# Performance work log

Measured on AMD Instinct MI355X. Metric: run time of the kernel, lower is better.

Reference implementation:

```python
import jax, jax.numpy as jnp
import numpy as np

C = 64       # class_number (from json groups)
D = 256      # out_dimension = predicted.shape[1]
N = 262144   # batch size


def setup_inputs() -> dict:
    key = jax.random.key(0)
    k1, k2, k3, k4 = jax.random.split(key, 4)
    predicted = jax.random.normal(k1, (N, D), dtype=jnp.float32)
    target = jax.random.randint(k2, (N,), 0, C)
    centroids = jax.random.normal(k3, (C, D), dtype=jnp.float32)
    # accumulated per-class distance sums are nonnegative (sqrt is applied)
    distances = jax.random.uniform(k4, (C, 1), dtype=jnp.float32) * float(N)
    # count = bincount(target) as the torch module accumulates; clamp >= 1
    ones = jnp.ones((N,), jnp.float32)
    count = jnp.maximum(jax.ops.segment_sum(ones, target, num_segments=C), 1.0)[:, None]
    # build_class_weight_matrix: single group containing every label -> all 1.5
    class_weights = jnp.full((C, C), 1.5, dtype=jnp.float32)
    return dict(predicted=predicted, centroids=centroids, distances=distances,
                count=count, class_weights=class_weights, target=target)


def reference(predicted, centroids, distances, count, class_weights, target):
    # === calculate_loss path (epoch % 3 == 2) ===
    C_ = centroids.shape[0]
    sel_counts = count[target]            # [N,1] gather
    sel_centroids = centroids[target]     # [N,D] gather
    pr = predicted / sel_counts           # [N,D]
    cent_new = centroids.at[target].add(pr)                 # scatter-add
    vec = jnp.linalg.norm(sel_centroids - pr, axis=1)       # [N]
    s = distances.at[target].add(vec[:, None])              # scatter-add [C,1]
    s = jnp.sqrt(s) / count                                 # [C,1]
    # cdist(cent_new, cent_new, p=2) via the norm trick
    sq = jnp.sum(cent_new * cent_new, axis=1)               # [C]
    d2 = jnp.maximum(sq[:, None] + sq[None, :] - 2.0 * (cent_new @ cent_new.T), 0.0)
    mask = ~jnp.eye(C_, dtype=bool)
    m = jnp.sqrt(jnp.where(mask, d2, 1.0))                  # safe off-diagonal sqrt
    S = s + s.T                                             # s[i] + s[j], [C,C]
    term = jnp.where(mask, class_weights * S / m, 0.0)
    sum_ = jnp.sum(term)
    loss = sum_ / C_ * (C_ - 1)
    return loss + jnp.sum(jnp.abs(cent_new)) / 1000000.0
```

## Files before the change

kernel.cpp:

```cpp
#include <hip/hip_runtime.h>
#include <math.h>

#define NROWS 262144
#define DIM   256
#define NC    64
#define CD    (NC*DIM)
#define NBLK  512

#define OFF_CENT   0
#define OFF_ABS    16384
#define OFF_PAIR   16896
#define OFF_SPART  16960
#define OFF_SST2   49728
#define OFF_PART   50752

typedef short  bf16x8 __attribute__((ext_vector_type(8)));
typedef float  f32x16 __attribute__((ext_vector_type(16)));

#define DPP_ADD(v, ctrl) \
    ((v) + __int_as_float(__builtin_amdgcn_update_dpp(0, __float_as_int(v), (ctrl), 0xf, 0xf, true)))

__device__ __forceinline__ float dpp_sum64(float v) {
    v = DPP_ADD(v, 0x111);
    v = DPP_ADD(v, 0x112);
    v = DPP_ADD(v, 0x114);
    v = DPP_ADD(v, 0x118);
    v = DPP_ADD(v, 0x142);
    v = DPP_ADD(v, 0x143);
    return v;
}

__device__ __forceinline__ unsigned int bf16rne2(float lo, float hi) {
    unsigned int ul = __float_as_uint(lo);
    ul = (ul + 0x7FFFu + ((ul >> 16) & 1u)) >> 16;
    unsigned int uh = __float_as_uint(hi);
    uh = (uh + 0x7FFFu + ((uh >> 16) & 1u)) & 0xFFFF0000u;
    return ul | uh;
}
__device__ __forceinline__ unsigned short bf16rne1(float v) {
    unsigned int x = __float_as_uint(v);
    return (unsigned short)((x + 0x7FFFu + ((x >> 16) & 1u)) >> 16);
}
__device__ __forceinline__ float bflo(unsigned int u) { return __uint_as_float(u << 16); }
__device__ __forceinline__ float bfhi(unsigned int u) { return __uint_as_float(u & 0xFFFF0000u); }
__device__ __forceinline__ float bfup(unsigned short u) { return __uint_as_float(((unsigned int)u) << 16); }

__device__ __forceinline__ void do_mfma_chunk(const unsigned short* pb,
                                              const int* tgts, int rbase,
                                              int lane, int d0,
                                              f32x16& a0r, f32x16& a1r)
{
    const int g8  = (lane >> 5) << 3;
    const int cA  = lane & 31;
    const int cB  = 32 + cA;
    const int col = d0 + cA;
    #pragma unroll
    for (int ks = 0; ks < 4; ++ks) {
        const int rA = rbase + ks * 16 + g8;
        const int t0 = tgts[rA+0], t1 = tgts[rA+1], t2 = tgts[rA+2], t3 = tgts[rA+3];
        const int t4 = tgts[rA+4], t5 = tgts[rA+5], t6 = tgts[rA+6], t7 = tgts[rA+7];
        union { unsigned int u[4]; bf16x8 v; } A0, A1, B;
        A0.u[0] = ((t0==cA)?0x3F80u:0u) | (((t1==cA)?0x3F80u:0u) << 16);
        A0.u[1] = ((t2==cA)?0x3F80u:0u) | (((t3==cA)?0x3F80u:0u) << 16);
        A0.u[2] = ((t4==cA)?0x3F80u:0u) | (((t5==cA)?0x3F80u:0u) << 16);
        A0.u[3] = ((t6==cA)?0x3F80u:0u) | (((t7==cA)?0x3F80u:0u) << 16);
        A1.u[0] = ((t0==cB)?0x3F80u:0u) | (((t1==cB)?0x3F80u:0u) << 16);
        A1.u[1] = ((t2==cB)?0x3F80u:0u) | (((t3==cB)?0x3F80u:0u) << 16);
        A1.u[2] = ((t4==cB)?0x3F80u:0u) | (((t5==cB)?0x3F80u:0u) << 16);
        A1.u[3] = ((t6==cB)?0x3F80u:0u) | (((t7==cB)?0x3F80u:0u) << 16);
        const int kr = ks * 16 + g8;
        #pragma unroll
        for (int p = 0; p < 4; ++p) {
            const unsigned int lo = pb[(kr + 2*p    ) * 256 + col];
            const unsigned int hi = pb[(kr + 2*p + 1) * 256 + col];
            B.u[p] = lo | (hi << 16);
        }
        a0r = __builtin_amdgcn_mfma_f32_32x32x16_bf16(A0.v, B.v, a0r, 0, 0, 0);
        a1r = __builtin_amdgcn_mfma_f32_32x32x16_bf16(A1.v, B.v, a1r, 0, 0, 0);
    }
}

__global__ __launch_bounds__(512, 4)
void k_main(const float* __restrict__ pred, const float* __restrict__ cent,
            const float* __restrict__ count, const int* __restrict__ tgt,
            float* __restrict__ ws)
{
    __shared__ unsigned short pbf[64 * 256];
    __shared__ unsigned short cbf[NC * 256];
    __shared__ int   tgt_s[512];
    __shared__ float inv_s[64];
    __shared__ float vec_s[512];
    __shared__ float sw_s[8][64];

    const int tid  = threadIdx.x;
    const int w    = tid >> 6;
    const int lane = tid & 63;
    const int base = blockIdx.x * 512;

    tgt_s[tid] = tgt[base + tid];
    if (tid < 64) inv_s[tid] = 1.0f / count[tid];
    {
        const float2* c2 = (const float2*)cent;
        unsigned int* cb32 = (unsigned int*)cbf;
        #pragma unroll
        for (int i = 0; i < 16; ++i) {
            const int o = i * 512 + tid;
            const float2 cf = c2[o];
            cb32[o] = bf16rne2(cf.x, cf.y);
        }
    }
    __syncthreads();

    const float4* pred4 = (const float4*)pred;
    const int d0 = w * 32;

    f32x16 acc0 = {};
    f32x16 acc1 = {};

    #pragma unroll 1
    for (int ch = 0; ch < 8; ++ch) {
        const size_t gr = (size_t)(base + ch * 64) * 64 + lane;
        float4 p0 = pred4[gr + (size_t)( 0 + w) * 64];
        float4 p1 = pred4[gr + (size_t)( 8 + w) * 64];
        float4 p2 = pred4[gr + (size_t)(16 + w) * 64];
        float4 p3 = pred4[gr + (size_t)(24 + w) * 64];
        float4 p4 = pred4[gr + (size_t)(32 + w) * 64];
        float4 p5 = pred4[gr + (size_t)(40 + w) * 64];
        float4 p6 = pred4[gr + (size_t)(48 + w) * 64];
        float4 p7 = pred4[gr + (size_t)(56 + w) * 64];

#define ROW(pp, i)                                                             \
        {                                                                      \
            const int rc = 8*(i) + w;                                          \
            const int r  = ch * 64 + rc;                                       \
            const int c  = tgt_s[r];                                           \
            const float iv = inv_s[c];                                         \
            const uint2 cu = *(const uint2*)&cbf[c * 256 + lane * 4];          \
            const float dx = bflo(cu.x) - pp.x * iv;                           \
            const float dy = bfhi(cu.x) - pp.y * iv;                           \
            const float dz = bflo(cu.y) - pp.z * iv;                           \
            const float dw = bfhi(cu.y) - pp.w * iv;                           \
            float ss = dx*dx + dy*dy + dz*dz + dw*dw;                          \
            ss = dpp_sum64(ss);                                                \
            if (lane == 63) vec_s[r] = sqrtf(ss);                              \
            *(uint2*)&pbf[rc * 256 + lane * 4] =                               \
                make_uint2(bf16rne2(pp.x, pp.y), bf16rne2(pp.z, pp.w));        \
        }
        ROW(p0, 0) ROW(p1, 1) ROW(p2, 2) ROW(p3, 3)
        ROW(p4, 4) ROW(p5, 5) ROW(p6, 6) ROW(p7, 7)
#undef ROW
        __syncthreads();
        do_mfma_chunk(pbf, tgt_s, ch * 64, lane, d0, acc0, acc1);
        __syncthreads();
    }

    unsigned short* pp = (unsigned short*)(ws + OFF_PART) + (size_t)blockIdx.x * CD;
    const int dim = d0 + (lane & 31);
    #pragma unroll
    for (int reg = 0; reg < 16; ++reg) {
        const int crow = (reg & 3) + 8 * (reg >> 2) + 4 * (lane >> 5);
        pp[(     crow) * 256 + dim] = bf16rne1(acc0[reg]);
        pp[(32 + crow) * 256 + dim] = bf16rne1(acc1[reg]);
    }

    {
        const float vv = vec_s[w * 64 + lane];
        const int   cc = tgt_s[w * 64 + lane];
        float accs = 0.f;
        for (int k = 0; k < NC; ++k) {
            float sel = (cc == k) ? vv : 0.f;
            sel = dpp_sum64(sel);
            const float tot = __shfl(sel, 63, 64);
            accs += (lane == k) ? tot : 0.f;
        }
        sw_s[w][lane] = accs;
    }
    __syncthreads();
    if (w == 0) {
        float s = 0.f;
        #pragma unroll
        for (int q = 0; q < 8; ++q) s += sw_s[q][lane];
        ws[OFF_SPART + blockIdx.x * 64 + lane] = s;
    }
}

__global__ __launch_bounds__(512)
void k_red2(const float* __restrict__ cent, const float* __restrict__ count,
            float* __restrict__ ws)
{
    __shared__ float red2[16][32];
    __shared__ float absl[32];
    __shared__ float sred[8][64];
    const int b = blockIdx.x, tid = threadIdx.x;

    const int eo = tid & 31;
    const int g  = tid >> 5;
    const int e  = b * 32 + eo;
    const unsigned short* pp = (const unsigned short*)(ws + OFF_PART);
    float s = 0.f;
    const int p0 = g * 32;
    #pragma unroll 8
    for (int p = p0; p < p0 + 32; ++p) s += bfup(pp[(size_t)p * CD + e]);
    red2[g][eo] = s;
    __syncthreads();
    if (tid < 32) {
        float tot = 0.f;
        #pragma unroll
        for (int q = 0; q < 16; ++q) tot += red2[q][tid];
        const int e2 = b * 32 + tid;
        const int c  = e2 >> 8;
        const float val = cent[e2] + tot / count[c];
        ws[OFF_CENT + e2] = val;
        absl[tid] = fabsf(val);
    }
    __syncthreads();
    if (tid < 64) {
        float a = (tid < 32) ? absl[tid] : 0.f;
        a = dpp_sum64(a);
        if (tid == 63) ws[OFF_ABS + b] = a;
    }
    if (b >= 496) {
        const int q  = b - 496;
        const int c  = tid & 63;
        const int rw = tid >> 6;
        float s2 = 0.f;
        #pragma unroll
        for (int i = 0; i < 4; ++i)
            s2 += ws[OFF_SPART + (q * 32 + rw * 4 + i) * 64 + c];
        sred[rw][c] = s2;
        __syncthreads();
        if (tid < 64) {
            float sv = 0.f;
            #pragma unroll
            for (int r = 0; r < 8; ++r) sv += sred[r][tid];
            ws[OFF_SST2 + q * 64 + tid] = sv;
        }
    }
}

__global__ __launch_bounds__(512)
void k_pairs(const float* __restrict__ count, const float* __restrict__ dist,
             const float* __restrict__ cw, float* __restrict__ ws)
{
    __shared__ float sf_s[64];
    __shared__ float wsum[8];
    const int i = blockIdx.x, tid = threadIdx.x;
    const int w = tid >> 6, lane = tid & 63;

    if (tid < 64) {
        float sv = 0.f;
        #pragma unroll
        for (int q = 0; q < 16; ++q) sv += ws[OFF_SST2 + q * 64 + tid];
        sf_s[tid] = sqrtf(dist[tid] + sv) / count[tid];
    }
    __syncthreads();
    const float4* c4 = (const float4*)(ws + OFF_CENT);
    const float si = sf_s[i];
    const float4 ci = c4[i * 64 + lane];
    float acc = 0.f;
    for (int j = w; j < NC; j += 8) {
        if (j == i) continue;
        const float4 cj = c4[j * 64 + lane];
        const float dx = ci.x - cj.x, dy = ci.y - cj.y;
        const float dz = ci.z - cj.z, dw = ci.w - cj.w;
        float ss = dx*dx + dy*dy + dz*dz + dw*dw;
        ss = dpp_sum64(ss);
        if (lane == 63) acc += cw[i * NC + j] * (si + sf_s[j]) / sqrtf(ss);
    }
    if (lane == 63) wsum[w] = acc;
    __syncthreads();
    if (tid == 0) {
        float ps = 0.f;
        #pragma unroll
        for (int q = 0; q < 8; ++q) ps += wsum[q];
        ws[OFF_PAIR + i] = ps;
    }
}

__global__ __launch_bounds__(512)
void k_fin(const float* __restrict__ ws, float* __restrict__ out)
{
    __shared__ float ra[8], rp[8];
    const int tid = threadIdx.x, w = tid >> 6, lane = tid & 63;
    float a = ws[OFF_ABS + tid];
    float p = (tid < 64) ? ws[OFF_PAIR + tid] : 0.f;
    a = dpp_sum64(a);
    p = dpp_sum64(p);
    if (lane == 63) { ra[w] = a; rp[w] = p; }
    __syncthreads();
    if (tid == 0) {
        float as = 0.f, ps = 0.f;
        #pragma unroll
        for (int q = 0; q < 8; ++q) { as += ra[q]; ps += rp[q]; }
        out[0] = ps / 64.0f * 63.0f + as * 1e-6f;
    }
}

extern "C" void kernel_launch(void* const* d_in, const int* in_sizes, int n_in,
                              void* d_out, int out_size, void* d_ws, size_t ws_size,
                              hipStream_t stream)
{
    const float* pred  = (const float*)d_in[0];
    const float* cent  = (const float*)d_in[1];
    const float* dist  = (const float*)d_in[2];
    const float* count = (const float*)d_in[3];
    const float* cw    = (const float*)d_in[4];
    const int*   tgt   = (const int*)d_in[5];
    float* ws  = (float*)d_ws;
    float* out = (float*)d_out;

    k_main <<<NBLK, 512, 0, stream>>>(pred, cent, count, tgt, ws);
    k_red2 <<<NBLK, 512, 0, stream>>>(cent, count, ws);
    k_pairs<<<NC,   512, 0, stream>>>(count, dist, cw, ws);
    k_fin  <<<1,    512, 0, stream>>>(ws, out);
}
```

Before: 75.03 us.

## Double-buffer LDS tiles and prefetch next chunk to overlap loads with MFMA

```diff
diff --git a/kernel.cpp b/kernel.cpp
--- a/kernel.cpp
+++ b/kernel.cpp
@@ -45,17 +45,25 @@
 __device__ __forceinline__ float bfhi(unsigned int u) { return __uint_as_float(u & 0xFFFF0000u); }
 __device__ __forceinline__ float bfup(unsigned short u) { return __uint_as_float(((unsigned int)u) << 16); }
 
-__device__ __forceinline__ void do_mfma_chunk(const unsigned short* pb,
-                                              const int* tgts, int rbase,
-                                              int lane, int d0,
-                                              f32x16& a0r, f32x16& a1r)
+__device__ __forceinline__ void lds_barrier() {
+    __builtin_amdgcn_sched_barrier(0);
+    asm volatile("s_waitcnt lgkmcnt(0)" ::: "memory");
+    __builtin_amdgcn_sched_barrier(0);
+    __builtin_amdgcn_s_barrier();
+    __builtin_amdgcn_sched_barrier(0);
+}
+
+__device__ __forceinline__ void do_mfma_chunk32(const unsigned short* pb,
+                                                const int* tgts, int rbase,
+                                                int lane, int d0,
+                                                f32x16& a0r, f32x16& a1r)
 {
     const int g8  = (lane >> 5) << 3;
     const int cA  = lane & 31;
     const int cB  = 32 + cA;
     const int col = d0 + cA;
     #pragma unroll
-    for (int ks = 0; ks < 4; ++ks) {
+    for (int ks = 0; ks < 2; ++ks) {
         const int rA = rbase + ks * 16 + g8;
         const int t0 = tgts[rA+0], t1 = tgts[rA+1], t2 = tgts[rA+2], t3 = tgts[rA+3];
         const int t4 = tgts[rA+4], t5 = tgts[rA+5], t6 = tgts[rA+6], t7 = tgts[rA+7];
@@ -68,7 +76,7 @@
         A1.u[1] = ((t2==cB)?0x3F80u:0u) | (((t3==cB)?0x3F80u:0u) << 16);
         A1.u[2] = ((t4==cB)?0x3F80u:0u) | (((t5==cB)?0x3F80u:0u) << 16);
         A1.u[3] = ((t6==cB)?0x3F80u:0u) | (((t7==cB)?0x3F80u:0u) << 16);
-        const int kr = ks * 16 + g8;
+        const int kr = (ks * 16 + g8) & 31;
         #pragma unroll
         for (int p = 0; p < 4; ++p) {
             const unsigned int lo = pb[(kr + 2*p    ) * 256 + col];
@@ -85,7 +93,7 @@
             const float* __restrict__ count, const int* __restrict__ tgt,
             float* __restrict__ ws)
 {
-    __shared__ unsigned short pbf[64 * 256];
+    __shared__ unsigned short pbf[2][32 * 256];
     __shared__ unsigned short cbf[NC * 256];
     __shared__ int   tgt_s[512];
     __shared__ float inv_s[64];
@@ -117,22 +125,19 @@
     f32x16 acc0 = {};
     f32x16 acc1 = {};
 
-    #pragma unroll 1
-    for (int ch = 0; ch < 8; ++ch) {
-        const size_t gr = (size_t)(base + ch * 64) * 64 + lane;
-        float4 p0 = pred4[gr + (size_t)( 0 + w) * 64];
-        float4 p1 = pred4[gr + (size_t)( 8 + w) * 64];
-        float4 p2 = pred4[gr + (size_t)(16 + w) * 64];
-        float4 p3 = pred4[gr + (size_t)(24 + w) * 64];
-        float4 p4 = pred4[gr + (size_t)(32 + w) * 64];
-        float4 p5 = pred4[gr + (size_t)(40 + w) * 64];
-        float4 p6 = pred4[gr + (size_t)(48 + w) * 64];
-        float4 p7 = pred4[gr + (size_t)(56 + w) * 64];
-
-#define ROW(pp, i)                                                             \
+    float4 p0, p1, p2, p3;
+
+#define LOADCH(cc) {                                                           \
+        const size_t gr = (size_t)(base + (cc) * 32) * 64 + lane;              \
+        p0 = pred4[gr + (size_t)( 0 + w) * 64];                                \
+        p1 = pred4[gr + (size_t)( 8 + w) * 64];                                \
+        p2 = pred4[gr + (size_t)(16 + w) * 64];                                \
+        p3 = pred4[gr + (size_t)(24 + w) * 64]; }
+
+#define ROWQ(pp, i, bsel, cc)                                                  \
         {                                                                      \
             const int rc = 8*(i) + w;                                          \
-            const int r  = ch * 64 + rc;                                       \
+            const int r  = (cc) * 32 + rc;                                     \
             const int c  = tgt_s[r];                                           \
             const float iv = inv_s[c];                                         \
             const uint2 cu = *(const uint2*)&cbf[c * 256 + lane * 4];          \
@@ -143,16 +148,33 @@
             float ss = dx*dx + dy*dy + dz*dz + dw*dw;                          \
             ss = dpp_sum64(ss);                                                \
             if (lane == 63) vec_s[r] = sqrtf(ss);                              \
-            *(uint2*)&pbf[rc * 256 + lane * 4] =                               \
+            *(uint2*)&pbf[bsel][rc * 256 + lane * 4] =                         \
                 make_uint2(bf16rne2(pp.x, pp.y), bf16rne2(pp.z, pp.w));        \
         }
-        ROW(p0, 0) ROW(p1, 1) ROW(p2, 2) ROW(p3, 3)
-        ROW(p4, 4) ROW(p5, 5) ROW(p6, 6) ROW(p7, 7)
-#undef ROW
-        __syncthreads();
-        do_mfma_chunk(pbf, tgt_s, ch * 64, lane, d0, acc0, acc1);
-        __syncthreads();
-    }
+
+#define ROWS4(bsel, cc)                                                        \
+        ROWQ(p0, 0, bsel, cc) ROWQ(p1, 1, bsel, cc)                            \
+        ROWQ(p2, 2, bsel, cc) ROWQ(p3, 3, bsel, cc)
+
+    LOADCH(0)
+    ROWS4(0, 0)
+    LOADCH(1)
+    lds_barrier();
+
+    int cur = 0;
+    #pragma unroll 1
+    for (int ch = 0; ch < 16; ++ch) {
+        if (ch < 15) {
+            ROWS4(cur ^ 1, ch + 1)
+            if (ch < 14) LOADCH(ch + 2)
+        }
+        do_mfma_chunk32(pbf[cur], tgt_s, ch * 32, lane, d0, acc0, acc1);
+        lds_barrier();
+        cur ^= 1;
+    }
+#undef LOADCH
+#undef ROWQ
+#undef ROWS4
 
     unsigned short* pp = (unsigned short*)(ws + OFF_PART) + (size_t)blockIdx.x * CD;
     const int dim = d0 + (lane & 31);
@@ -163,6 +185,7 @@
         pp[(32 + crow) * 256 + dim] = bf16rne1(acc1[reg]);
     }
 
+    __syncthreads();
     {
         const float vv = vec_s[w * 64 + lane];
         const int   cc = tgt_s[w * 64 + lane];
```

New measurement: 77.48 us. 3.3% more time.
